# Optimization experiments

Hardware: AMD Instinct MI355X
Metric: run time of the kernel (lower is better)

Reference implementation:

```python
import jax, jax.numpy as jnp
import numpy as np

D = 1024
H = 16
HD = D // H
C = 50000


def setup_inputs() -> dict:
    key = jax.random.key(0)
    ks = jax.random.split(key, 16)
    s = 0.02
    return {
        "nodes": jax.random.normal(ks[0], (C, D), dtype=jnp.float32),
        "z_prev": jax.random.normal(ks[1], (D,), dtype=jnp.float32),
        "Wq": jax.random.normal(ks[2], (D, D), dtype=jnp.float32) * s,
        "bq": jnp.zeros((D,), dtype=jnp.float32),
        "Wk": jax.random.normal(ks[3], (D, D), dtype=jnp.float32) * s,
        "bk": jnp.zeros((D,), dtype=jnp.float32),
        "Wv": jax.random.normal(ks[4], (D, D), dtype=jnp.float32) * s,
        "bv": jnp.zeros((D,), dtype=jnp.float32),
        "W1": jax.random.normal(ks[5], (2 * D, D), dtype=jnp.float32) * s,
        "b1": jnp.zeros((D,), dtype=jnp.float32),
        "W2": jax.random.normal(ks[6], (D, D), dtype=jnp.float32) * s,
        "b2": jnp.zeros((D,), dtype=jnp.float32),
        "scale": jnp.ones((D,), dtype=jnp.float32),
    }


def _rmsnorm(x, scale, eps=1e-6):
    # matches torch: scale * x * rsqrt(mean(x^2) + eps)
    ms = jnp.mean(jnp.square(x), axis=-1, keepdims=True)
    return scale * x * jax.lax.rsqrt(ms + eps)


def reference(nodes, z_prev, Wq, bq, Wk, bk, Wv, bv, W1, b1, W2, b2, scale):
    # projections (weights stored [in, out])
    Q = (z_prev @ Wq + bq).reshape(H, HD)          # [H, hd]
    K = (nodes @ Wk + bk).reshape(C, H, HD)        # [C, H, hd]
    V = (nodes @ Wv + bv).reshape(C, H, HD)        # [C, H, hd]
    # single-query multi-head attention over C nodes
    scores = jnp.einsum("hd,chd->hc", Q, K) / np.sqrt(HD).astype(np.float32)
    weights = jax.nn.softmax(scores, axis=-1)      # [H, C]
    pooled = jnp.einsum("hc,chd->hd", weights, V).reshape(D)
    # concat -> MLP (GELU exact, matching torch nn.GELU default) -> RMSNorm
    z = jnp.concatenate([pooled, z_prev], axis=-1)  # [2D]
    h = jax.nn.gelu(z @ W1 + b1, approximate=False)
    z_out = _rmsnorm(h @ W2 + b2, scale)
    return z_out
```

## Files before the change

kernel.cpp:

```cpp
#include <hip/hip_runtime.h>
#include <hip/hip_bf16.h>
#include <math.h>

#define C_N 50000

typedef float f32x16 __attribute__((ext_vector_type(16)));
typedef float f32x4v __attribute__((ext_vector_type(4)));
typedef short bf16x8 __attribute__((ext_vector_type(8)));
typedef unsigned short u16x4 __attribute__((ext_vector_type(4)));
typedef unsigned short u16x2 __attribute__((ext_vector_type(2)));
#define VZERO16 {0.f,0.f,0.f,0.f,0.f,0.f,0.f,0.f,0.f,0.f,0.f,0.f,0.f,0.f,0.f,0.f}

#define OQ     0
#define OZ     1024
#define OH     3072
#define OY     4096
#define OSUMB  5120
#define OQKB   13312
#define OPP2   21504
#define OPP    283648

__device__ __forceinline__ int brev4(int l){
  return ((l&1)<<3)|((l&2)<<1)|((l&4)>>1)|((l&8)>>3);
}

__device__ __forceinline__ float bf2f(unsigned short u){
  unsigned int x = ((unsigned int)u)<<16;
  return __builtin_bit_cast(float, x);
}

__device__ __forceinline__ float vred16(f32x16 v, int lane){
  float send, got;
#define RS(A,B,M) \
  send = (lane&M)? v[A] : v[B]; \
  got  = __shfl_xor(send, M);   \
  v[A] = ((lane&M)? v[B] : v[A]) + got;
  RS(0,8,1) RS(1,9,1) RS(2,10,1) RS(3,11,1)
  RS(4,12,1) RS(5,13,1) RS(6,14,1) RS(7,15,1)
  RS(0,4,2) RS(1,5,2) RS(2,6,2) RS(3,7,2)
  RS(0,2,4) RS(1,3,4)
  RS(0,1,8)
#undef RS
  float t = v[0];
  t += __shfl_xor(t,16);
  t += __shfl_xor(t,32);
  return t;
}

template<int IN, int NT>
__device__ __forceinline__ float mv_dot(const float* __restrict__ W,
    const float* __restrict__ x, int tid, int jblk){
  __shared__ float xs[IN];
  __shared__ float red[NT/16][17];
  for (int k=tid;k<IN;k+=NT) xs[k]=x[k];
  __syncthreads();
  int jq = tid&15, iq = tid>>4;
  int j = jblk*16 + jq;
  float acc = 0.f;
#pragma unroll 8
  for (int i=iq;i<IN;i+=NT/16)
    acc = fmaf(xs[i], W[(size_t)i*1024 + j], acc);
  red[iq][jq] = acc;
  __syncthreads();
  float s = 0.f;
  if (tid < 16){
#pragma unroll
    for (int ii=0;ii<NT/16;ii++) s += red[ii][tid];
  }
  return s;
}

__global__ __launch_bounds__(1024) void hm_mvQ(const float* __restrict__ W,
    const float* __restrict__ x, const float* __restrict__ bq,
    float* __restrict__ Q, float* __restrict__ z){
  float s = mv_dot<1024,1024>(W, x, threadIdx.x, blockIdx.x);
  int tid = threadIdx.x;
  int j0 = blockIdx.x*16;
  if (tid < 16){
    Q[j0+tid] = s + bq[j0+tid];
    z[1024 + j0 + tid] = x[j0 + tid];
  }
}

__global__ __launch_bounds__(256) void hm_qk2(const float* __restrict__ Wk,
    const float* __restrict__ Q, unsigned short* __restrict__ qkb){
  __shared__ float qlds[1024];
  int tid = threadIdx.x;
  for (int k=tid;k<1024;k+=256) qlds[k]=Q[k];
  __syncthreads();
  int w = tid>>6, l = tid&63;
  int i = blockIdx.x*4 + w;
  const float* wr = Wk + (size_t)i*1024 + l;
  f32x16 acc = VZERO16;
#define QKS(k) acc[k] = wr[k*64] * qlds[k*64 + l];
  QKS(0) QKS(1) QKS(2) QKS(3) QKS(4) QKS(5) QKS(6) QKS(7)
  QKS(8) QKS(9) QKS(10) QKS(11) QKS(12) QKS(13) QKS(14) QKS(15)
#undef QKS
  float t = vred16(acc, l);
  if (l < 16){
    int h = brev4(l);
    int kc = i>>5, rg = (i>>3)&3, jj = i&7;
    __hip_bfloat16 b = __float2bfloat16(t);
    qkb[(kc*64 + rg*16 + h)*8 + jj] = *(unsigned short*)&b;
  }
}

#define LD2(AP,KC,FA,FB) \
  FA = *(const float4*)((AP)+(KC)*32); \
  FB = *(const float4*)((AP)+(KC)*32+4);
#define CVT8(FA,FB,AV) { \
  __hip_bfloat16 c0=__float2bfloat16(FA.x),c1=__float2bfloat16(FA.y); \
  __hip_bfloat16 c2=__float2bfloat16(FA.z),c3=__float2bfloat16(FA.w); \
  __hip_bfloat16 c4=__float2bfloat16(FB.x),c5=__float2bfloat16(FB.y); \
  __hip_bfloat16 c6=__float2bfloat16(FB.z),c7=__float2bfloat16(FB.w); \
  AV[0]=*(short*)&c0; AV[1]=*(short*)&c1; AV[2]=*(short*)&c2; AV[3]=*(short*)&c3; \
  AV[4]=*(short*)&c4; AV[5]=*(short*)&c5; AV[6]=*(short*)&c6; AV[7]=*(short*)&c7; }

__global__ __launch_bounds__(256,2) void hm_fused(const float* __restrict__ nodes,
    const unsigned short* __restrict__ qkb, unsigned short* __restrict__ parts,
    float* __restrict__ sumpb){
  extern __shared__ float tile[];
  __shared__ float part[4][16][17];
  __shared__ float eb[16][16];
  const int tid = threadIdx.x, w = tid>>6, l = tid&63;
  const int rowA = l&15, kgrp = l>>4;
  const int r_ = tid>>4, h_ = tid&15;

  bf16x8 bq0,bq1,bq2,bq3,bq4,bq5,bq6,bq7;
  {
    const bf16x8* qb = (const bf16x8*)qkb;
    const int o = w*8*64 + l;
    bq0=qb[o]; bq1=qb[o+64]; bq2=qb[o+128]; bq3=qb[o+192];
    bq4=qb[o+256]; bq5=qb[o+320]; bq6=qb[o+384]; bq7=qb[o+448];
  }
  f32x16 a0 = VZERO16, a1 = VZERO16, a2 = VZERO16, a3 = VZERO16;
  float ssum = 0.f;
  const int stride = gridDim.x;

  int cb = blockIdx.x;
  float4 p0a,p0b,p1a,p1b,p2a,p2b,p3a,p3b,p4a,p4b,p5a,p5b,p6a,p6b,p7a,p7b;
  {
    const float* ap = nodes + ((size_t)(cb*16 + rowA))*1024 + w*256 + kgrp*8;
    LD2(ap,0,p0a,p0b) LD2(ap,1,p1a,p1b) LD2(ap,2,p2a,p2b) LD2(ap,3,p3a,p3b)
    LD2(ap,4,p4a,p4b) LD2(ap,5,p5a,p5b) LD2(ap,6,p6a,p6b) LD2(ap,7,p7a,p7b)
  }
  float* tw = tile + rowA*1028 + w*256 + kgrp*8;

  for (; cb < 3125; cb += stride){
    __syncthreads();
    *(float4*)(tw+0*32) = p0a; *(float4*)(tw+0*32+4) = p0b;
    *(float4*)(tw+1*32) = p1a; *(float4*)(tw+1*32+4) = p1b;
    *(float4*)(tw+2*32) = p2a; *(float4*)(tw+2*32+4) = p2b;
    *(float4*)(tw+3*32) = p3a; *(float4*)(tw+3*32+4) = p3b;
    *(float4*)(tw+4*32) = p4a; *(float4*)(tw+4*32+4) = p4b;
    *(float4*)(tw+5*32) = p5a; *(float4*)(tw+5*32+4) = p5b;
    *(float4*)(tw+6*32) = p6a; *(float4*)(tw+6*32+4) = p6b;
    *(float4*)(tw+7*32) = p7a; *(float4*)(tw+7*32+4) = p7b;
    bf16x8 av0,av1,av2,av3,av4,av5,av6,av7;
    CVT8(p0a,p0b,av0) CVT8(p1a,p1b,av1) CVT8(p2a,p2b,av2) CVT8(p3a,p3b,av3)
    CVT8(p4a,p4b,av4) CVT8(p5a,p5b,av5) CVT8(p6a,p6b,av6) CVT8(p7a,p7b,av7)
    f32x4v D0 = {0.f,0.f,0.f,0.f};
    f32x4v D1 = {0.f,0.f,0.f,0.f};
    D0 = __builtin_amdgcn_mfma_f32_16x16x32_bf16(av0, bq0, D0, 0,0,0);
    D1 = __builtin_amdgcn_mfma_f32_16x16x32_bf16(av1, bq1, D1, 0,0,0);
    D0 = __builtin_amdgcn_mfma_f32_16x16x32_bf16(av2, bq2, D0, 0,0,0);
    D1 = __builtin_amdgcn_mfma_f32_16x16x32_bf16(av3, bq3, D1, 0,0,0);
    D0 = __builtin_amdgcn_mfma_f32_16x16x32_bf16(av4, bq4, D0, 0,0,0);
    D1 = __builtin_amdgcn_mfma_f32_16x16x32_bf16(av5, bq5, D1, 0,0,0);
    D0 = __builtin_amdgcn_mfma_f32_16x16x32_bf16(av6, bq6, D0, 0,0,0);
    D1 = __builtin_amdgcn_mfma_f32_16x16x32_bf16(av7, bq7, D1, 0,0,0);
    {
      int cbn = cb + stride; if (cbn >= 3125) cbn = cb;
      const float* apn = nodes + ((size_t)(cbn*16 + rowA))*1024 + w*256 + kgrp*8;
      LD2(apn,0,p0a,p0b) LD2(apn,1,p1a,p1b) LD2(apn,2,p2a,p2b) LD2(apn,3,p3a,p3b)
      LD2(apn,4,p4a,p4b) LD2(apn,5,p5a,p5b) LD2(apn,6,p6a,p6b) LD2(apn,7,p7a,p7b)
    }
#pragma unroll
    for (int i=0;i<4;i++) part[w][kgrp*4+i][rowA] = D0[i] + D1[i];
    __syncthreads();
    {
      float s = part[0][r_][h_]+part[1][r_][h_]+part[2][r_][h_]+part[3][r_][h_];
      eb[r_][h_] = __expf(s * 0.125f);
    }
    __syncthreads();
    if (tid < 16){
#pragma unroll
      for (int rr=0;rr<16;rr++) ssum += eb[rr][tid];
    }
    const float* tr = tile + w*256 + l*4;
#pragma unroll 4
    for (int r=0;r<16;r++){
      float4 nv = *(const float4*)(tr + r*1028);
      f32x16 u = *(const f32x16*)&eb[r][0];
      a0 += u*nv.x; a1 += u*nv.y; a2 += u*nv.z; a3 += u*nv.w;
    }
  }
  unsigned short* p = parts + (size_t)blockIdx.x*16384 + w*256 + l*4;
#pragma unroll
  for (int h=0;h<16;h++){
    __hip_bfloat16 b0=__float2bfloat16(a0[h]), b1=__float2bfloat16(a1[h]);
    __hip_bfloat16 b2=__float2bfloat16(a2[h]), b3=__float2bfloat16(a3[h]);
    u16x4 o;
    o[0]=*(unsigned short*)&b0; o[1]=*(unsigned short*)&b1;
    o[2]=*(unsigned short*)&b2; o[3]=*(unsigned short*)&b3;
    *(u16x4*)(p + h*1024) = o;
  }
  if (tid < 16) sumpb[blockIdx.x*16 + tid] = ssum;
}

__global__ __launch_bounds__(256) void hm_predA(const unsigned short* __restrict__ parts,
    unsigned short* __restrict__ pp2, int nb){
  int j2 = blockIdx.x*256 + threadIdx.x;
  int b0 = blockIdx.y*16;
  int b1 = b0+16 < nb ? b0+16 : nb;
  float s0 = 0.f, s1 = 0.f;
  for (int b=b0;b<b1;b++){
    u16x2 v = *(const u16x2*)&parts[(size_t)b*16384 + j2*2];
    s0 += bf2f(v[0]); s1 += bf2f(v[1]);
  }
  __hip_bfloat16 r0=__float2bfloat16(s0), r1=__float2bfloat16(s1);
  u16x2 o; o[0]=*(unsigned short*)&r0; o[1]=*(unsigned short*)&r1;
  *(u16x2*)&pp2[(size_t)blockIdx.y*16384 + j2*2] = o;
}

__global__ __launch_bounds__(1024) void hm_mvV(const float* __restrict__ W,
    const unsigned short* __restrict__ pp2, const float* __restrict__ sumpb,
    const float* __restrict__ bv, float* __restrict__ z, int ny, int nb){
  __shared__ float xs[1024];
  __shared__ float red[64][17];
  __shared__ float ssl[16];
  const int tid = threadIdx.x;
  const int hh = blockIdx.x>>2;
  float sacc = 0.f;
  for (int b=tid; b<nb; b+=1024) sacc += sumpb[b*16 + hh];
#pragma unroll
  for (int m=1;m<64;m<<=1) sacc += __shfl_xor(sacc, m);
  if ((tid&63)==0) ssl[tid>>6] = sacc;
  {
    int k = tid;
    float s = 0.f;
    for (int y=0;y<ny;y++) s += bf2f(pp2[(size_t)y*16384 + hh*1024 + k]);
    xs[k] = s;
  }
  __syncthreads();
  int jq = tid&15, iq = tid>>4;
  int j = blockIdx.x*16 + jq;
  float acc = 0.f;
#pragma unroll 8
  for (int i=iq;i<1024;i+=64)
    acc = fmaf(xs[i], W[(size_t)i*1024 + j], acc);
  red[iq][jq] = acc;
  __syncthreads();
  if (tid < 16){
    float s = 0.f;
#pragma unroll
    for (int ii=0;ii<64;ii++) s += red[ii][tid];
    float S = 0.f;
#pragma unroll
    for (int q=0;q<16;q++) S += ssl[q];
    int jo = blockIdx.x*16 + tid;
    z[jo] = s / S + bv[jo];
  }
}

__global__ __launch_bounds__(1024) void hm_mvW1(const float* __restrict__ W,
    const float* __restrict__ z, const float* __restrict__ b1,
    float* __restrict__ hbuf){
  float s = mv_dot<2048,1024>(W, z, threadIdx.x, blockIdx.x);
  int tid = threadIdx.x;
  if (tid < 16){
    int j = blockIdx.x*16 + tid;
    float v = s + b1[j];
    hbuf[j] = 0.5f * v * (1.0f + erff(v * 0.70710678118654752f));
  }
}

__global__ __launch_bounds__(1024) void hm_mvW2(const float* __restrict__ W,
    const float* __restrict__ hb, const float* __restrict__ b2,
    float* __restrict__ y){
  float s = mv_dot<1024,1024>(W, hb, threadIdx.x, blockIdx.x);
  int tid = threadIdx.x;
  if (tid < 16){
    int j = blockIdx.x*16 + tid;
    y[j] = s + b2[j];
  }
}

__global__ __launch_bounds__(256) void hm_rms(const float* __restrict__ y,
    const float* __restrict__ scale, float* __restrict__ out){
  __shared__ float red[4];
  __shared__ float msv;
  int tid = threadIdx.x;
  float local = 0.f;
  for (int j=tid;j<1024;j+=256){ float t = y[j]; local = fmaf(t,t,local); }
#pragma unroll
  for (int m=1;m<64;m<<=1) local += __shfl_xor(local, m);
  if ((tid&63)==0) red[tid>>6] = local;
  __syncthreads();
  if (tid==0){
    float s = red[0]+red[1]+red[2]+red[3];
    msv = rsqrtf(s*(1.0f/1024.0f) + 1e-6f);
  }
  __syncthreads();
  float r = msv;
  for (int j=tid;j<1024;j+=256) out[j] = scale[j]*y[j]*r;
}

extern "C" void kernel_launch(void* const* d_in, const int* in_sizes, int n_in,
                              void* d_out, int out_size, void* d_ws, size_t ws_size,
                              hipStream_t stream){
  const float* nodes  = (const float*)d_in[0];
  const float* z_prev = (const float*)d_in[1];
  const float* Wq = (const float*)d_in[2];
  const float* bq = (const float*)d_in[3];
  const float* Wk = (const float*)d_in[4];
  const float* Wv = (const float*)d_in[6];
  const float* bv = (const float*)d_in[7];
  const float* W1 = (const float*)d_in[8];
  const float* b1 = (const float*)d_in[9];
  const float* W2 = (const float*)d_in[10];
  const float* b2 = (const float*)d_in[11];
  const float* scale = (const float*)d_in[12];
  float* ws  = (float*)d_ws;
  float* out = (float*)d_out;

  float* Qv   = ws + OQ;
  float* z    = ws + OZ;
  float* hbuf = ws + OH;
  float* ybuf = ws + OY;
  float* sumb = ws + OSUMB;
  unsigned short* qkb = (unsigned short*)(ws + OQKB);
  unsigned short* pp2 = (unsigned short*)(ws + OPP2);
  unsigned short* pp  = (unsigned short*)(ws + OPP);

  size_t need0 = (size_t)OPP*4;
  int nbp = 1;
  if (ws_size > need0 + 32768) nbp = (int)((ws_size - need0)/32768);
  if (nbp > 512) nbp = 512;
  if (nbp < 1) nbp = 1;
  int ny = (nbp + 15)/16;

  const size_t tile_bytes = 16*1028*sizeof(float);

  hm_mvQ   <<<64,  1024, 0, stream>>>(Wq, z_prev, bq, Qv, z);
  hm_qk2   <<<256, 256, 0, stream>>>(Wk, Qv, qkb);
  hm_fused <<<nbp, 256, tile_bytes, stream>>>(nodes, qkb, pp, sumb);
  hm_predA <<<dim3(32,ny), 256, 0, stream>>>(pp, pp2, nbp);
  hm_mvV   <<<64,  1024, 0, stream>>>(Wv, pp2, sumb, bv, z, ny, nbp);
  hm_mvW1  <<<64,  1024, 0, stream>>>(W1, z, b1, hbuf);
  hm_mvW2  <<<64,  1024, 0, stream>>>(W2, hbuf, b2, ybuf);
  hm_rms   <<<1,   256, 0, stream>>>(ybuf, scale, out);
}
```

Baseline: 89.65 us.

## Merge small GEMV and reduction kernels into two cooperative grid-synced kernels

Replaces the Q projection and Q·Wk kernels with one cooperative kernel that splits the input dimension across 256 blocks and uses a grid sync. It also replaces the partial-sum reduction, V, W1 and W2 matvecs and RMSNorm with one cooperative tail kernel that separates its phases with grid syncs. The aim is to cut launch overhead and the serialization of many tiny kernels, and to spread each GEMV across more blocks. In exchange it adds grid-wide barrier cost. The block count for the fused kernel is now rounded to a multiple of 16, which the new reduction requires.

```diff
diff --git a/kernel.cpp b/kernel.cpp
--- a/kernel.cpp
+++ b/kernel.cpp
@@ -1,6 +1,9 @@
 #include <hip/hip_runtime.h>
 #include <hip/hip_bf16.h>
+#include <hip/hip_cooperative_groups.h>
 #include <math.h>
+
+namespace cg = cooperative_groups;
 
 #define C_N 50000
 
@@ -11,14 +14,15 @@
 typedef unsigned short u16x2 __attribute__((ext_vector_type(2)));
 #define VZERO16 {0.f,0.f,0.f,0.f,0.f,0.f,0.f,0.f,0.f,0.f,0.f,0.f,0.f,0.f,0.f,0.f}
 
-#define OQ     0
-#define OZ     1024
-#define OH     3072
-#define OY     4096
-#define OSUMB  5120
-#define OQKB   13312
-#define OPP2   21504
-#define OPP    283648
+#define OQP    0
+#define OSUMB  4096
+#define OQKB   12288
+#define OSS    20480
+#define OZP    20496
+#define OH1P   24592
+#define OY2P   28688
+#define OPA    32784
+#define OPP    294928
 
 __device__ __forceinline__ int brev4(int l){
   return ((l&1)<<3)|((l&2)<<1)|((l&4)>>1)|((l&8)>>3);
@@ -47,49 +51,45 @@
   return t;
 }
 
-template<int IN, int NT>
-__device__ __forceinline__ float mv_dot(const float* __restrict__ W,
-    const float* __restrict__ x, int tid, int jblk){
-  __shared__ float xs[IN];
-  __shared__ float red[NT/16][17];
-  for (int k=tid;k<IN;k+=NT) xs[k]=x[k];
-  __syncthreads();
-  int jq = tid&15, iq = tid>>4;
-  int j = jblk*16 + jq;
-  float acc = 0.f;
-#pragma unroll 8
-  for (int i=iq;i<IN;i+=NT/16)
-    acc = fmaf(xs[i], W[(size_t)i*1024 + j], acc);
-  red[iq][jq] = acc;
-  __syncthreads();
-  float s = 0.f;
-  if (tid < 16){
-#pragma unroll
-    for (int ii=0;ii<NT/16;ii++) s += red[ii][tid];
-  }
-  return s;
-}
-
-__global__ __launch_bounds__(1024) void hm_mvQ(const float* __restrict__ W,
-    const float* __restrict__ x, const float* __restrict__ bq,
-    float* __restrict__ Q, float* __restrict__ z){
-  float s = mv_dot<1024,1024>(W, x, threadIdx.x, blockIdx.x);
-  int tid = threadIdx.x;
-  int j0 = blockIdx.x*16;
-  if (tid < 16){
-    Q[j0+tid] = s + bq[j0+tid];
-    z[1024 + j0 + tid] = x[j0 + tid];
-  }
-}
-
-__global__ __launch_bounds__(256) void hm_qk2(const float* __restrict__ Wk,
-    const float* __restrict__ Q, unsigned short* __restrict__ qkb){
+__global__ __launch_bounds__(256) void hm_front(const float* __restrict__ Wq,
+    const float* __restrict__ z_prev, const float* __restrict__ bq,
+    const float* __restrict__ Wk, float* __restrict__ qp,
+    unsigned short* __restrict__ qkb){
+  __shared__ float xs[256];
+  __shared__ float red[16][17];
   __shared__ float qlds[1024];
-  int tid = threadIdx.x;
-  for (int k=tid;k<1024;k+=256) qlds[k]=Q[k];
+  const int tid = threadIdx.x, bid = blockIdx.x;
+  {
+    int jblk = bid>>2, iseg = bid&3;
+    xs[tid] = z_prev[iseg*256 + tid];
+    __syncthreads();
+    int jq = tid&15, iq = tid>>4;
+    const float* Wp = Wq + (size_t)(iseg*256)*1024 + jblk*16 + jq;
+    float acc = 0.f;
+#pragma unroll
+    for (int k=0;k<16;k++){
+      int il = iq + 16*k;
+      acc = fmaf(xs[il], Wp[(size_t)il*1024], acc);
+    }
+    red[iq][jq] = acc;
+    __syncthreads();
+    if (tid < 16){
+      float s = 0.f;
+#pragma unroll
+      for (int ii=0;ii<16;ii++) s += red[ii][tid];
+      qp[iseg*1024 + jblk*16 + tid] = s;
+    }
+  }
+  cg::this_grid().sync();
+  for (int k=tid;k<1024;k+=256){
+    float q = bq[k];
+#pragma unroll
+    for (int s=0;s<4;s++) q += qp[s*1024 + k];
+    qlds[k] = q;
+  }
   __syncthreads();
   int w = tid>>6, l = tid&63;
-  int i = blockIdx.x*4 + w;
+  int i = bid*4 + w;
   const float* wr = Wk + (size_t)i*1024 + l;
   f32x16 acc = VZERO16;
 #define QKS(k) acc[k] = wr[k*64] * qlds[k*64 + l];
@@ -208,102 +208,158 @@
   if (tid < 16) sumpb[blockIdx.x*16 + tid] = ssum;
 }
 
-__global__ __launch_bounds__(256) void hm_predA(const unsigned short* __restrict__ parts,
-    unsigned short* __restrict__ pp2, int nb){
-  int j2 = blockIdx.x*256 + threadIdx.x;
-  int b0 = blockIdx.y*16;
-  int b1 = b0+16 < nb ? b0+16 : nb;
-  float s0 = 0.f, s1 = 0.f;
-  for (int b=b0;b<b1;b++){
-    u16x2 v = *(const u16x2*)&parts[(size_t)b*16384 + j2*2];
-    s0 += bf2f(v[0]); s1 += bf2f(v[1]);
-  }
-  __hip_bfloat16 r0=__float2bfloat16(s0), r1=__float2bfloat16(s1);
-  u16x2 o; o[0]=*(unsigned short*)&r0; o[1]=*(unsigned short*)&r1;
-  *(u16x2*)&pp2[(size_t)blockIdx.y*16384 + j2*2] = o;
-}
-
-__global__ __launch_bounds__(1024) void hm_mvV(const float* __restrict__ W,
-    const unsigned short* __restrict__ pp2, const float* __restrict__ sumpb,
-    const float* __restrict__ bv, float* __restrict__ z, int ny, int nb){
-  __shared__ float xs[1024];
-  __shared__ float red[64][17];
-  __shared__ float ssl[16];
-  const int tid = threadIdx.x;
-  const int hh = blockIdx.x>>2;
-  float sacc = 0.f;
-  for (int b=tid; b<nb; b+=1024) sacc += sumpb[b*16 + hh];
-#pragma unroll
-  for (int m=1;m<64;m<<=1) sacc += __shfl_xor(sacc, m);
-  if ((tid&63)==0) ssl[tid>>6] = sacc;
-  {
-    int k = tid;
-    float s = 0.f;
-    for (int y=0;y<ny;y++) s += bf2f(pp2[(size_t)y*16384 + hh*1024 + k]);
-    xs[k] = s;
-  }
-  __syncthreads();
-  int jq = tid&15, iq = tid>>4;
-  int j = blockIdx.x*16 + jq;
-  float acc = 0.f;
-#pragma unroll 8
-  for (int i=iq;i<1024;i+=64)
-    acc = fmaf(xs[i], W[(size_t)i*1024 + j], acc);
-  red[iq][jq] = acc;
-  __syncthreads();
-  if (tid < 16){
-    float s = 0.f;
-#pragma unroll
-    for (int ii=0;ii<64;ii++) s += red[ii][tid];
-    float S = 0.f;
-#pragma unroll
-    for (int q=0;q<16;q++) S += ssl[q];
-    int jo = blockIdx.x*16 + tid;
-    z[jo] = s / S + bv[jo];
-  }
-}
-
-__global__ __launch_bounds__(1024) void hm_mvW1(const float* __restrict__ W,
-    const float* __restrict__ z, const float* __restrict__ b1,
-    float* __restrict__ hbuf){
-  float s = mv_dot<2048,1024>(W, z, threadIdx.x, blockIdx.x);
-  int tid = threadIdx.x;
-  if (tid < 16){
-    int j = blockIdx.x*16 + tid;
-    float v = s + b1[j];
-    hbuf[j] = 0.5f * v * (1.0f + erff(v * 0.70710678118654752f));
-  }
-}
-
-__global__ __launch_bounds__(1024) void hm_mvW2(const float* __restrict__ W,
-    const float* __restrict__ hb, const float* __restrict__ b2,
-    float* __restrict__ y){
-  float s = mv_dot<1024,1024>(W, hb, threadIdx.x, blockIdx.x);
-  int tid = threadIdx.x;
-  if (tid < 16){
-    int j = blockIdx.x*16 + tid;
-    y[j] = s + b2[j];
-  }
-}
-
-__global__ __launch_bounds__(256) void hm_rms(const float* __restrict__ y,
-    const float* __restrict__ scale, float* __restrict__ out){
-  __shared__ float red[4];
+__global__ __launch_bounds__(512) void hm_tail(
+    const unsigned short* __restrict__ pp, const float* __restrict__ sumpb,
+    float* __restrict__ pA, float* __restrict__ S,
+    float* __restrict__ zpart, float* __restrict__ h1part,
+    float* __restrict__ y2part,
+    const float* __restrict__ Wv, const float* __restrict__ bv,
+    const float* __restrict__ z_prev,
+    const float* __restrict__ W1, const float* __restrict__ b1,
+    const float* __restrict__ W2, const float* __restrict__ b2,
+    const float* __restrict__ scale, float* __restrict__ out, int nb){
+  __shared__ float xs[512];
+  __shared__ float red[32][17];
+  __shared__ float yb[1024];
+  __shared__ float rr[8];
   __shared__ float msv;
-  int tid = threadIdx.x;
-  float local = 0.f;
-  for (int j=tid;j<1024;j+=256){ float t = y[j]; local = fmaf(t,t,local); }
-#pragma unroll
-  for (int m=1;m<64;m<<=1) local += __shfl_xor(local, m);
-  if ((tid&63)==0) red[tid>>6] = local;
-  __syncthreads();
-  if (tid==0){
-    float s = red[0]+red[1]+red[2]+red[3];
-    msv = rsqrtf(s*(1.0f/1024.0f) + 1e-6f);
-  }
-  __syncthreads();
-  float r = msv;
-  for (int j=tid;j<1024;j+=256) out[j] = scale[j]*y[j]*r;
+  const int tid = threadIdx.x, bid = blockIdx.x;
+  {
+    int gtid = bid*512 + tid;
+    int seg = gtid>>13, j2 = gtid&8191;
+    int cnt = nb>>4;
+    float s0=0.f, s1=0.f;
+    for (int b=seg*cnt; b<(seg+1)*cnt; b++){
+      u16x2 v = *(const u16x2*)&pp[(size_t)b*16384 + j2*2];
+      s0 += bf2f(v[0]); s1 += bf2f(v[1]);
+    }
+    float2 o = make_float2(s0,s1);
+    *(float2*)&pA[(size_t)seg*16384 + j2*2] = o;
+    if (bid == 0){
+      int h = tid&15, g = tid>>4;
+      float sp = 0.f;
+      for (int b=g; b<nb; b+=32) sp += sumpb[b*16 + h];
+      red[g][h] = sp;
+      __syncthreads();
+      if (tid < 16){
+        float sv=0.f;
+#pragma unroll
+        for (int gg=0; gg<32; gg++) sv += red[gg][tid];
+        S[tid] = sv;
+      }
+    }
+  }
+  cg::this_grid().sync();
+  {
+    int jblk = bid>>2, iseg = bid&3, hh = jblk>>2;
+    if (tid < 256){
+      float s = 0.f;
+      int base = hh*1024 + iseg*256 + tid;
+#pragma unroll
+      for (int sg=0; sg<16; sg++) s += pA[(size_t)sg*16384 + base];
+      xs[tid] = s;
+    }
+    __syncthreads();
+    int jq = tid&15, iq = tid>>4;
+    const float* Wp = Wv + (size_t)(iseg*256)*1024 + jblk*16 + jq;
+    float acc = 0.f;
+#pragma unroll
+    for (int k=0;k<8;k++){
+      int il = iq + 32*k;
+      acc = fmaf(xs[il], Wp[(size_t)il*1024], acc);
+    }
+    red[iq][jq] = acc;
+    __syncthreads();
+    if (tid < 16){
+      float s=0.f;
+#pragma unroll
+      for (int ii=0;ii<32;ii++) s += red[ii][tid];
+      zpart[iseg*1024 + jblk*16 + tid] = s;
+    }
+  }
+  cg::this_grid().sync();
+  {
+    int jblk = bid>>2, iseg = bid&3;
+    int jj = iseg*512 + tid;
+    float xv;
+    if (jj < 1024){
+      float s = 0.f;
+#pragma unroll
+      for (int sg=0; sg<4; sg++) s += zpart[sg*1024 + jj];
+      xv = s / S[jj>>6] + bv[jj];
+    } else {
+      xv = z_prev[jj-1024];
+    }
+    xs[tid] = xv;
+    __syncthreads();
+    int jq = tid&15, iq = tid>>4;
+    const float* Wp = W1 + (size_t)(iseg*512)*1024 + jblk*16 + jq;
+    float acc = 0.f;
+#pragma unroll
+    for (int k=0;k<16;k++){
+      int il = iq + 32*k;
+      acc = fmaf(xs[il], Wp[(size_t)il*1024], acc);
+    }
+    red[iq][jq] = acc;
+    __syncthreads();
+    if (tid < 16){
+      float s=0.f;
+#pragma unroll
+      for (int ii=0;ii<32;ii++) s += red[ii][tid];
+      h1part[iseg*1024 + jblk*16 + tid] = s;
+    }
+  }
+  cg::this_grid().sync();
+  {
+    int jblk = bid>>2, iseg = bid&3;
+    __syncthreads();
+    if (tid < 256){
+      int ii = iseg*256 + tid;
+      float s = b1[ii];
+#pragma unroll
+      for (int sg=0; sg<4; sg++) s += h1part[sg*1024 + ii];
+      xs[tid] = 0.5f * s * (1.0f + erff(s * 0.70710678118654752f));
+    }
+    __syncthreads();
+    int jq = tid&15, iq = tid>>4;
+    const float* Wp = W2 + (size_t)(iseg*256)*1024 + jblk*16 + jq;
+    float acc = 0.f;
+#pragma unroll
+    for (int k=0;k<8;k++){
+      int il = iq + 32*k;
+      acc = fmaf(xs[il], Wp[(size_t)il*1024], acc);
+    }
+    red[iq][jq] = acc;
+    __syncthreads();
+    if (tid < 16){
+      float s=0.f;
+#pragma unroll
+      for (int ii=0;ii<32;ii++) s += red[ii][tid];
+      y2part[iseg*1024 + jblk*16 + tid] = s;
+    }
+  }
+  cg::this_grid().sync();
+  if (bid == 0){
+    float loc = 0.f;
+    for (int j=tid; j<1024; j+=512){
+      float y = b2[j];
+#pragma unroll
+      for (int sg=0; sg<4; sg++) y += y2part[sg*1024 + j];
+      yb[j] = y;
+      loc = fmaf(y,y,loc);
+    }
+#pragma unroll
+    for (int m=1;m<64;m<<=1) loc += __shfl_xor(loc, m);
+    if ((tid&63)==0) rr[tid>>6] = loc;
+    __syncthreads();
+    if (tid==0){
+      float s = rr[0]+rr[1]+rr[2]+rr[3]+rr[4]+rr[5]+rr[6]+rr[7];
+      msv = rsqrtf(s*(1.0f/1024.0f) + 1e-6f);
+    }
+    __syncthreads();
+    float r = msv;
+    for (int j=tid;j<1024;j+=512) out[j] = scale[j]*yb[j]*r;
+  }
 }
 
 extern "C" void kernel_launch(void* const* d_in, const int* in_sizes, int n_in,
@@ -324,30 +380,43 @@
   float* ws  = (float*)d_ws;
   float* out = (float*)d_out;
 
-  float* Qv   = ws + OQ;
-  float* z    = ws + OZ;
-  float* hbuf = ws + OH;
-  float* ybuf = ws + OY;
-  float* sumb = ws + OSUMB;
+  float* qp     = ws + OQP;
+  float* sumb   = ws + OSUMB;
   unsigned short* qkb = (unsigned short*)(ws + OQKB);
-  unsigned short* pp2 = (unsigned short*)(ws + OPP2);
-  unsigned short* pp  = (unsigned short*)(ws + OPP);
-
-  size_t need0 = (size_t)OPP*4;
-  int nbp = 1;
-  if (ws_size > need0 + 32768) nbp = (int)((ws_size - need0)/32768);
-  if (nbp > 512) nbp = 512;
-  if (nbp < 1) nbp = 1;
-  int ny = (nbp + 15)/16;
+  float* Sv     = ws + OSS;
+  float* zpart  = ws + OZP;
+  float* h1part = ws + OH1P;
+  float* y2part = ws + OY2P;
+  float* pA     = ws + OPA;
+  unsigned short* pp = (unsigned short*)(ws + OPP);
+
+  int nbp = 512;
+  {
+    size_t avail_f = ws_size/4;
+    if (avail_f > (size_t)OPP){
+      size_t cap = (avail_f - OPP)/8192;
+      if ((size_t)nbp > cap) nbp = (int)cap;
+    } else nbp = 16;
+    nbp &= ~15;
+    if (nbp < 16) nbp = 16;
+  }
 
   const size_t tile_bytes = 16*1028*sizeof(float);
 
-  hm_mvQ   <<<64,  1024, 0, stream>>>(Wq, z_prev, bq, Qv, z);
-  hm_qk2   <<<256, 256, 0, stream>>>(Wk, Qv, qkb);
-  hm_fused <<<nbp, 256, tile_bytes, stream>>>(nodes, qkb, pp, sumb);
-  hm_predA <<<dim3(32,ny), 256, 0, stream>>>(pp, pp2, nbp);
-  hm_mvV   <<<64,  1024, 0, stream>>>(Wv, pp2, sumb, bv, z, ny, nbp);
-  hm_mvW1  <<<64,  1024, 0, stream>>>(W1, z, b1, hbuf);
-  hm_mvW2  <<<64,  1024, 0, stream>>>(W2, hbuf, b2, ybuf);
-  hm_rms   <<<1,   256, 0, stream>>>(ybuf, scale, out);
-}
+  {
+    void* fargs[] = {(void*)&Wq, (void*)&z_prev, (void*)&bq, (void*)&Wk,
+                     (void*)&qp, (void*)&qkb};
+    hipLaunchCooperativeKernel((const void*)hm_front, dim3(256), dim3(256),
+                               fargs, 0, stream);
+  }
+  hm_fused<<<nbp, 256, tile_bytes, stream>>>(nodes, qkb, pp, sumb);
+  {
+    void* targs[] = {(void*)&pp, (void*)&sumb, (void*)&pA, (void*)&Sv,
+                     (void*)&zpart, (void*)&h1part, (void*)&y2part,
+                     (void*)&Wv, (void*)&bv, (void*)&z_prev,
+                     (void*)&W1, (void*)&b1, (void*)&W2, (void*)&b2,
+                     (void*)&scale, (void*)&out, (void*)&nbp};
+    hipLaunchCooperativeKernel((const void*)hm_tail, dim3(256), dim3(512),
+                               targs, 0, stream);
+  }
+}
```

Measured after the change: 229.0 us. 2.55x slower.

## Split W1 matvec over K, fold GELU into W2, widen predA loads

Applied to the files above, without the earlier changes.

The W1 matvec now runs on a 2D grid that splits the 2048-long input into two 1024 segments. It writes two partial sums, and the W2 kernel adds them together with b1 and applies GELU while staging its input, which doubles the block count for the W1 stage. The partial-reduction kernel reads and writes four bf16 values per thread instead of two and uses half as many blocks. The top-of-loop __syncthreads in the fused attention kernel is removed. That drops a barrier per tile but risks a write-after-read race on the shared tile if no other barrier guards it.

```diff
diff --git a/kernel.cpp b/kernel.cpp
--- a/kernel.cpp
+++ b/kernel.cpp
@@ -8,17 +8,16 @@
 typedef float f32x4v __attribute__((ext_vector_type(4)));
 typedef short bf16x8 __attribute__((ext_vector_type(8)));
 typedef unsigned short u16x4 __attribute__((ext_vector_type(4)));
-typedef unsigned short u16x2 __attribute__((ext_vector_type(2)));
 #define VZERO16 {0.f,0.f,0.f,0.f,0.f,0.f,0.f,0.f,0.f,0.f,0.f,0.f,0.f,0.f,0.f,0.f}
 
 #define OQ     0
 #define OZ     1024
-#define OH     3072
-#define OY     4096
-#define OSUMB  5120
-#define OQKB   13312
-#define OPP2   21504
-#define OPP    283648
+#define OH1P   3072
+#define OY     5120
+#define OSUMB  6144
+#define OQKB   14336
+#define OPP2   22528
+#define OPP    284672
 
 __device__ __forceinline__ int brev4(int l){
   return ((l&1)<<3)|((l&2)<<1)|((l&4)>>1)|((l&8)>>3);
@@ -147,7 +146,6 @@
   float* tw = tile + rowA*1028 + w*256 + kgrp*8;
 
   for (; cb < 3125; cb += stride){
-    __syncthreads();
     *(float4*)(tw+0*32) = p0a; *(float4*)(tw+0*32+4) = p0b;
     *(float4*)(tw+1*32) = p1a; *(float4*)(tw+1*32+4) = p1b;
     *(float4*)(tw+2*32) = p2a; *(float4*)(tw+2*32+4) = p2b;
@@ -210,17 +208,20 @@
 
 __global__ __launch_bounds__(256) void hm_predA(const unsigned short* __restrict__ parts,
     unsigned short* __restrict__ pp2, int nb){
-  int j2 = blockIdx.x*256 + threadIdx.x;
+  int j4 = blockIdx.x*256 + threadIdx.x;
   int b0 = blockIdx.y*16;
   int b1 = b0+16 < nb ? b0+16 : nb;
-  float s0 = 0.f, s1 = 0.f;
+  float s0=0.f, s1=0.f, s2=0.f, s3=0.f;
   for (int b=b0;b<b1;b++){
-    u16x2 v = *(const u16x2*)&parts[(size_t)b*16384 + j2*2];
-    s0 += bf2f(v[0]); s1 += bf2f(v[1]);
+    u16x4 v = *(const u16x4*)&parts[(size_t)b*16384 + j4*4];
+    s0 += bf2f(v[0]); s1 += bf2f(v[1]); s2 += bf2f(v[2]); s3 += bf2f(v[3]);
   }
   __hip_bfloat16 r0=__float2bfloat16(s0), r1=__float2bfloat16(s1);
-  u16x2 o; o[0]=*(unsigned short*)&r0; o[1]=*(unsigned short*)&r1;
-  *(u16x2*)&pp2[(size_t)blockIdx.y*16384 + j2*2] = o;
+  __hip_bfloat16 r2=__float2bfloat16(s2), r3=__float2bfloat16(s3);
+  u16x4 o;
+  o[0]=*(unsigned short*)&r0; o[1]=*(unsigned short*)&r1;
+  o[2]=*(unsigned short*)&r2; o[3]=*(unsigned short*)&r3;
+  *(u16x4*)&pp2[(size_t)blockIdx.y*16384 + j4*4] = o;
 }
 
 __global__ __launch_bounds__(1024) void hm_mvV(const float* __restrict__ W,
@@ -264,25 +265,59 @@
 }
 
 __global__ __launch_bounds__(1024) void hm_mvW1(const float* __restrict__ W,
-    const float* __restrict__ z, const float* __restrict__ b1,
-    float* __restrict__ hbuf){
-  float s = mv_dot<2048,1024>(W, z, threadIdx.x, blockIdx.x);
-  int tid = threadIdx.x;
-  if (tid < 16){
-    int j = blockIdx.x*16 + tid;
-    float v = s + b1[j];
-    hbuf[j] = 0.5f * v * (1.0f + erff(v * 0.70710678118654752f));
+    const float* __restrict__ z, float* __restrict__ h1part){
+  __shared__ float xs[1024];
+  __shared__ float red[64][17];
+  const int tid = threadIdx.x;
+  const int iseg = blockIdx.y;
+  xs[tid] = z[iseg*1024 + tid];
+  __syncthreads();
+  int jq = tid&15, iq = tid>>4;
+  int j = blockIdx.x*16 + jq;
+  const float* Wp = W + (size_t)(iseg*1024)*1024;
+  float acc = 0.f;
+#pragma unroll
+  for (int k=0;k<16;k++){
+    int i = iq + 64*k;
+    acc = fmaf(xs[i], Wp[(size_t)i*1024 + j], acc);
+  }
+  red[iq][jq] = acc;
+  __syncthreads();
+  if (tid < 16){
+    float s = 0.f;
+#pragma unroll
+    for (int ii=0;ii<64;ii++) s += red[ii][tid];
+    h1part[iseg*1024 + blockIdx.x*16 + tid] = s;
   }
 }
 
 __global__ __launch_bounds__(1024) void hm_mvW2(const float* __restrict__ W,
-    const float* __restrict__ hb, const float* __restrict__ b2,
-    float* __restrict__ y){
-  float s = mv_dot<1024,1024>(W, hb, threadIdx.x, blockIdx.x);
-  int tid = threadIdx.x;
-  if (tid < 16){
-    int j = blockIdx.x*16 + tid;
-    y[j] = s + b2[j];
+    const float* __restrict__ h1part, const float* __restrict__ b1,
+    const float* __restrict__ b2, float* __restrict__ y){
+  __shared__ float xs[1024];
+  __shared__ float red[64][17];
+  const int tid = threadIdx.x;
+  {
+    float s = b1[tid] + h1part[tid] + h1part[1024 + tid];
+    xs[tid] = 0.5f * s * (1.0f + erff(s * 0.70710678118654752f));
+  }
+  __syncthreads();
+  int jq = tid&15, iq = tid>>4;
+  int j = blockIdx.x*16 + jq;
+  float acc = 0.f;
+#pragma unroll
+  for (int k=0;k<16;k++){
+    int i = iq + 64*k;
+    acc = fmaf(xs[i], W[(size_t)i*1024 + j], acc);
+  }
+  red[iq][jq] = acc;
+  __syncthreads();
+  if (tid < 16){
+    float s = 0.f;
+#pragma unroll
+    for (int ii=0;ii<64;ii++) s += red[ii][tid];
+    int jo = blockIdx.x*16 + tid;
+    y[jo] = s + b2[jo];
   }
 }
 
@@ -324,11 +359,11 @@
   float* ws  = (float*)d_ws;
   float* out = (float*)d_out;
 
-  float* Qv   = ws + OQ;
-  float* z    = ws + OZ;
-  float* hbuf = ws + OH;
-  float* ybuf = ws + OY;
-  float* sumb = ws + OSUMB;
+  float* Qv     = ws + OQ;
+  float* z      = ws + OZ;
+  float* h1part = ws + OH1P;
+  float* ybuf   = ws + OY;
+  float* sumb   = ws + OSUMB;
   unsigned short* qkb = (unsigned short*)(ws + OQKB);
   unsigned short* pp2 = (unsigned short*)(ws + OPP2);
   unsigned short* pp  = (unsigned short*)(ws + OPP);
@@ -345,9 +380,9 @@
   hm_mvQ   <<<64,  1024, 0, stream>>>(Wq, z_prev, bq, Qv, z);
   hm_qk2   <<<256, 256, 0, stream>>>(Wk, Qv, qkb);
   hm_fused <<<nbp, 256, tile_bytes, stream>>>(nodes, qkb, pp, sumb);
-  hm_predA <<<dim3(32,ny), 256, 0, stream>>>(pp, pp2, nbp);
+  hm_predA <<<dim3(16,ny), 256, 0, stream>>>(pp, pp2, nbp);
   hm_mvV   <<<64,  1024, 0, stream>>>(Wv, pp2, sumb, bv, z, ny, nbp);
-  hm_mvW1  <<<64,  1024, 0, stream>>>(W1, z, b1, hbuf);
-  hm_mvW2  <<<64,  1024, 0, stream>>>(W2, hbuf, b2, ybuf);
+  hm_mvW1  <<<dim3(64,2), 1024, 0, stream>>>(W1, z, h1part);
+  hm_mvW2  <<<64,  1024, 0, stream>>>(W2, h1part, b1, b2, ybuf);
   hm_rms   <<<1,   256, 0, stream>>>(ybuf, scale, out);
 }
```

After: 87.49 us. 1.02x faster.

## Overlap W1 z_prev half with V projection, widen predA, drop loop barrier

Applied to the files above, without the earlier changes.

The W1 matvec is split in two. The half that multiplies z_prev now runs in extra blocks (blockIdx.y=1) of the V-projection kernel, in parallel with the Wv matvec. A smaller kernel then finishes the pooled half, adds the partial sum, bias and GELU, which shortens the serial chain of matvec launches. Separately, the partial-reduction kernel loads four bf16 per thread instead of two, using half as many blocks. The leading __syncthreads in the fused attention loop is also removed, which risks a race on the shared tile between iterations if no other barrier guards it.

```diff
diff --git a/kernel.cpp b/kernel.cpp
--- a/kernel.cpp
+++ b/kernel.cpp
@@ -8,13 +8,13 @@
 typedef float f32x4v __attribute__((ext_vector_type(4)));
 typedef short bf16x8 __attribute__((ext_vector_type(8)));
 typedef unsigned short u16x4 __attribute__((ext_vector_type(4)));
-typedef unsigned short u16x2 __attribute__((ext_vector_type(2)));
 #define VZERO16 {0.f,0.f,0.f,0.f,0.f,0.f,0.f,0.f,0.f,0.f,0.f,0.f,0.f,0.f,0.f,0.f}
 
 #define OQ     0
-#define OZ     1024
-#define OH     3072
-#define OY     4096
+#define OZB    1024
+#define OH1L   2048
+#define OH1    3072
+#define OYB    4096
 #define OSUMB  5120
 #define OQKB   13312
 #define OPP2   21504
@@ -72,13 +72,12 @@
 
 __global__ __launch_bounds__(1024) void hm_mvQ(const float* __restrict__ W,
     const float* __restrict__ x, const float* __restrict__ bq,
-    float* __restrict__ Q, float* __restrict__ z){
+    float* __restrict__ Q){
   float s = mv_dot<1024,1024>(W, x, threadIdx.x, blockIdx.x);
   int tid = threadIdx.x;
-  int j0 = blockIdx.x*16;
   if (tid < 16){
+    int j0 = blockIdx.x*16;
     Q[j0+tid] = s + bq[j0+tid];
-    z[1024 + j0 + tid] = x[j0 + tid];
   }
 }
 
@@ -147,7 +146,6 @@
   float* tw = tile + rowA*1028 + w*256 + kgrp*8;
 
   for (; cb < 3125; cb += stride){
-    __syncthreads();
     *(float4*)(tw+0*32) = p0a; *(float4*)(tw+0*32+4) = p0b;
     *(float4*)(tw+1*32) = p1a; *(float4*)(tw+1*32+4) = p1b;
     *(float4*)(tw+2*32) = p2a; *(float4*)(tw+2*32+4) = p2b;
@@ -210,79 +208,100 @@
 
 __global__ __launch_bounds__(256) void hm_predA(const unsigned short* __restrict__ parts,
     unsigned short* __restrict__ pp2, int nb){
-  int j2 = blockIdx.x*256 + threadIdx.x;
+  int j4 = blockIdx.x*256 + threadIdx.x;
   int b0 = blockIdx.y*16;
   int b1 = b0+16 < nb ? b0+16 : nb;
-  float s0 = 0.f, s1 = 0.f;
+  float s0=0.f, s1=0.f, s2=0.f, s3=0.f;
   for (int b=b0;b<b1;b++){
-    u16x2 v = *(const u16x2*)&parts[(size_t)b*16384 + j2*2];
-    s0 += bf2f(v[0]); s1 += bf2f(v[1]);
+    u16x4 v = *(const u16x4*)&parts[(size_t)b*16384 + j4*4];
+    s0 += bf2f(v[0]); s1 += bf2f(v[1]); s2 += bf2f(v[2]); s3 += bf2f(v[3]);
   }
   __hip_bfloat16 r0=__float2bfloat16(s0), r1=__float2bfloat16(s1);
-  u16x2 o; o[0]=*(unsigned short*)&r0; o[1]=*(unsigned short*)&r1;
-  *(u16x2*)&pp2[(size_t)blockIdx.y*16384 + j2*2] = o;
-}
-
-__global__ __launch_bounds__(1024) void hm_mvV(const float* __restrict__ W,
+  __hip_bfloat16 r2=__float2bfloat16(s2), r3=__float2bfloat16(s3);
+  u16x4 o;
+  o[0]=*(unsigned short*)&r0; o[1]=*(unsigned short*)&r1;
+  o[2]=*(unsigned short*)&r2; o[3]=*(unsigned short*)&r3;
+  *(u16x4*)&pp2[(size_t)blockIdx.y*16384 + j4*4] = o;
+}
+
+__global__ __launch_bounds__(1024) void hm_mvV(const float* __restrict__ Wv,
     const unsigned short* __restrict__ pp2, const float* __restrict__ sumpb,
-    const float* __restrict__ bv, float* __restrict__ z, int ny, int nb){
+    const float* __restrict__ bv, const float* __restrict__ z_prev,
+    const float* __restrict__ W1, float* __restrict__ zbuf,
+    float* __restrict__ h1low, int ny, int nb){
   __shared__ float xs[1024];
   __shared__ float red[64][17];
   __shared__ float ssl[16];
   const int tid = threadIdx.x;
-  const int hh = blockIdx.x>>2;
-  float sacc = 0.f;
-  for (int b=tid; b<nb; b+=1024) sacc += sumpb[b*16 + hh];
-#pragma unroll
-  for (int m=1;m<64;m<<=1) sacc += __shfl_xor(sacc, m);
-  if ((tid&63)==0) ssl[tid>>6] = sacc;
-  {
-    int k = tid;
+  const int jq = tid&15, iq = tid>>4;
+  if (blockIdx.y == 0){
+    const int hh = blockIdx.x>>2;
+    float sacc = 0.f;
+    for (int b=tid; b<nb; b+=1024) sacc += sumpb[b*16 + hh];
+#pragma unroll
+    for (int m=1;m<64;m<<=1) sacc += __shfl_xor(sacc, m);
+    if ((tid&63)==0) ssl[tid>>6] = sacc;
     float s = 0.f;
-    for (int y=0;y<ny;y++) s += bf2f(pp2[(size_t)y*16384 + hh*1024 + k]);
-    xs[k] = s;
-  }
-  __syncthreads();
-  int jq = tid&15, iq = tid>>4;
-  int j = blockIdx.x*16 + jq;
-  float acc = 0.f;
+    for (int y=0;y<ny;y++) s += bf2f(pp2[(size_t)y*16384 + hh*1024 + tid]);
+    xs[tid] = s;
+    __syncthreads();
+    int j = blockIdx.x*16 + jq;
+    float acc = 0.f;
 #pragma unroll 8
-  for (int i=iq;i<1024;i+=64)
-    acc = fmaf(xs[i], W[(size_t)i*1024 + j], acc);
-  red[iq][jq] = acc;
-  __syncthreads();
+    for (int i=iq;i<1024;i+=64)
+      acc = fmaf(xs[i], Wv[(size_t)i*1024 + j], acc);
+    red[iq][jq] = acc;
+    __syncthreads();
+    if (tid < 16){
+      float s2 = 0.f;
+#pragma unroll
+      for (int ii=0;ii<64;ii++) s2 += red[ii][tid];
+      float S = 0.f;
+#pragma unroll
+      for (int q=0;q<16;q++) S += ssl[q];
+      int jo = blockIdx.x*16 + tid;
+      zbuf[jo] = s2 / S + bv[jo];
+    }
+  } else {
+    xs[tid] = z_prev[tid];
+    __syncthreads();
+    int j = blockIdx.x*16 + jq;
+    const float* Wp = W1 + (size_t)1024*1024;
+    float acc = 0.f;
+#pragma unroll 8
+    for (int i=iq;i<1024;i+=64)
+      acc = fmaf(xs[i], Wp[(size_t)i*1024 + j], acc);
+    red[iq][jq] = acc;
+    __syncthreads();
+    if (tid < 16){
+      float s = 0.f;
+#pragma unroll
+      for (int ii=0;ii<64;ii++) s += red[ii][tid];
+      h1low[blockIdx.x*16 + tid] = s;
+    }
+  }
+}
+
+__global__ __launch_bounds__(1024) void hm_mvW1u(const float* __restrict__ W1,
+    const float* __restrict__ zbuf, const float* __restrict__ h1low,
+    const float* __restrict__ b1, float* __restrict__ h1buf){
+  float s = mv_dot<1024,1024>(W1, zbuf, threadIdx.x, blockIdx.x);
+  int tid = threadIdx.x;
   if (tid < 16){
-    float s = 0.f;
-#pragma unroll
-    for (int ii=0;ii<64;ii++) s += red[ii][tid];
-    float S = 0.f;
-#pragma unroll
-    for (int q=0;q<16;q++) S += ssl[q];
     int jo = blockIdx.x*16 + tid;
-    z[jo] = s / S + bv[jo];
-  }
-}
-
-__global__ __launch_bounds__(1024) void hm_mvW1(const float* __restrict__ W,
-    const float* __restrict__ z, const float* __restrict__ b1,
-    float* __restrict__ hbuf){
-  float s = mv_dot<2048,1024>(W, z, threadIdx.x, blockIdx.x);
+    float v = s + h1low[jo] + b1[jo];
+    h1buf[jo] = 0.5f * v * (1.0f + erff(v * 0.70710678118654752f));
+  }
+}
+
+__global__ __launch_bounds__(1024) void hm_mvW2(const float* __restrict__ W2,
+    const float* __restrict__ h1buf, const float* __restrict__ b2,
+    float* __restrict__ ybuf){
+  float s = mv_dot<1024,1024>(W2, h1buf, threadIdx.x, blockIdx.x);
   int tid = threadIdx.x;
   if (tid < 16){
-    int j = blockIdx.x*16 + tid;
-    float v = s + b1[j];
-    hbuf[j] = 0.5f * v * (1.0f + erff(v * 0.70710678118654752f));
-  }
-}
-
-__global__ __launch_bounds__(1024) void hm_mvW2(const float* __restrict__ W,
-    const float* __restrict__ hb, const float* __restrict__ b2,
-    float* __restrict__ y){
-  float s = mv_dot<1024,1024>(W, hb, threadIdx.x, blockIdx.x);
-  int tid = threadIdx.x;
-  if (tid < 16){
-    int j = blockIdx.x*16 + tid;
-    y[j] = s + b2[j];
+    int jo = blockIdx.x*16 + tid;
+    ybuf[jo] = s + b2[jo];
   }
 }
 
@@ -324,11 +343,12 @@
   float* ws  = (float*)d_ws;
   float* out = (float*)d_out;
 
-  float* Qv   = ws + OQ;
-  float* z    = ws + OZ;
-  float* hbuf = ws + OH;
-  float* ybuf = ws + OY;
-  float* sumb = ws + OSUMB;
+  float* Qv     = ws + OQ;
+  float* zbuf   = ws + OZB;
+  float* h1low  = ws + OH1L;
+  float* h1buf  = ws + OH1;
+  float* ybuf   = ws + OYB;
+  float* sumb   = ws + OSUMB;
   unsigned short* qkb = (unsigned short*)(ws + OQKB);
   unsigned short* pp2 = (unsigned short*)(ws + OPP2);
   unsigned short* pp  = (unsigned short*)(ws + OPP);
@@ -342,12 +362,13 @@
 
   const size_t tile_bytes = 16*1028*sizeof(float);
 
-  hm_mvQ   <<<64,  1024, 0, stream>>>(Wq, z_prev, bq, Qv, z);
+  hm_mvQ   <<<64,  1024, 0, stream>>>(Wq, z_prev, bq, Qv);
   hm_qk2   <<<256, 256, 0, stream>>>(Wk, Qv, qkb);
   hm_fused <<<nbp, 256, tile_bytes, stream>>>(nodes, qkb, pp, sumb);
-  hm_predA <<<dim3(32,ny), 256, 0, stream>>>(pp, pp2, nbp);
-  hm_mvV   <<<64,  1024, 0, stream>>>(Wv, pp2, sumb, bv, z, ny, nbp);
-  hm_mvW1  <<<64,  1024, 0, stream>>>(W1, z, b1, hbuf);
-  hm_mvW2  <<<64,  1024, 0, stream>>>(W2, hbuf, b2, ybuf);
+  hm_predA <<<dim3(16,ny), 256, 0, stream>>>(pp, pp2, nbp);
+  hm_mvV   <<<dim3(64,2), 1024, 0, stream>>>(Wv, pp2, sumb, bv, z_prev, W1,
+                                             zbuf, h1low, ny, nbp);
+  hm_mvW1u <<<64,  1024, 0, stream>>>(W1, zbuf, h1low, b1, h1buf);
+  hm_mvW2  <<<64,  1024, 0, stream>>>(W2, h1buf, b2, ybuf);
   hm_rms   <<<1,   256, 0, stream>>>(ybuf, scale, out);
 }
```

New measurement: 87.47 us. -2.4%, faster.
